# Kernel optimization log

Hardware: AMD Instinct MI355X
Metric: run time of the kernel (lower is better)

Reference implementation:

```python
import jax, jax.numpy as jnp
import numpy as np


def setup_inputs() -> dict:
    key = jax.random.key(0)
    k1, k2, k3 = jax.random.split(key, 3)
    B, C, Hg, Wg, Dg = 4, 12, 16, 16, 8
    H, W = 1024, 1024
    grid = jax.random.normal(k1, (B, C, Hg, Wg, Dg), dtype=jnp.float32)
    guide = jax.random.uniform(k2, (B, 1, H, W), dtype=jnp.float32)
    input_image = jax.random.normal(k3, (B, 3, H, W), dtype=jnp.float32)
    return {"grid": grid, "guide": guide, "input_image": input_image}


def reference(grid, guide, input_image):
    # grid: [B, C, Hg, Wg, Dg]; guide: [B,1,H,W]; input_image: [B,3,H,W]
    B, C, Hg, Wg, Dg = grid.shape
    H, W = input_image.shape[2], input_image.shape[3]
    dt = grid.dtype

    # depth coordinate from guide (matches torch: floor -> clamp, frac clamped to [0,1])
    g = guide[:, 0]                                   # [B,H,W]
    d_coords = g * (Dg - 1)
    d_lo = jnp.clip(jnp.floor(d_coords), 0, Dg - 1)
    d_lo_i = d_lo.astype(jnp.int32)
    d_hi_i = jnp.minimum(d_lo_i + 1, Dg - 1)
    d_w = jnp.clip(d_coords - d_lo, 0.0, 1.0)         # [B,H,W]

    # Spatial coords. NOTE: the torch code stacks [y, x] but grid_sample reads (x, y),
    # so row index i maps to the grid WIDTH axis and column j maps to the HEIGHT axis.
    # align_corners=True: x_pix = (x_norm+1)/2*(size-1).
    i_idx = jnp.arange(H, dtype=dt)
    j_idx = jnp.arange(W, dtype=dt)
    ww = i_idx / (H - 1) * (Wg - 1)                   # [H], width coord per row
    hh = j_idx / (W - 1) * (Hg - 1)                   # [W], height coord per col
    w0 = jnp.floor(ww).astype(jnp.int32)
    w1 = jnp.minimum(w0 + 1, Wg - 1)
    fw = ww - w0.astype(dt)                           # [H]
    h0 = jnp.floor(hh).astype(jnp.int32)
    h1 = jnp.minimum(h0 + 1, Hg - 1)
    fh = hh - h0.astype(dt)                           # [W]

    grid_t = jnp.transpose(grid, (0, 2, 3, 4, 1))     # [B,Hg,Wg,Dg,C]
    b = jnp.arange(B)[:, None, None]                  # [B,1,1]

    def corner(hI, wI, dI):
        # hI:[W] (col-dependent), wI:[H] (row-dependent), dI:[B,H,W]
        return grid_t[b, hI[None, None, :], wI[None, :, None], dI]  # [B,H,W,C]

    fh_b = fh[None, None, :, None]                    # [1,1,W,1]
    fw_b = fw[None, :, None, None]                    # [1,H,1,1]
    dw_b = d_w[..., None]                             # [B,H,W,1]

    out = jnp.zeros((B, H, W, C), dtype=dt)
    for hI, wh in ((h0, 1.0 - fh_b), (h1, fh_b)):
        for wI, wwt in ((w0, 1.0 - fw_b), (w1, fw_b)):
            for dI, wd in ((d_lo_i, 1.0 - dw_b), (d_hi_i, dw_b)):
                out = out + (wh * wwt * wd) * corner(hI, wI, dI)
    return jnp.transpose(out, (0, 3, 1, 2))           # [B,C,H,W]
```

## Files before the change

### kernel.cpp

```cpp
#include <hip/hip_runtime.h>

#define B_SZ 4
#define C_CH 12
#define H_G 16
#define W_G 16
#define D_G 8
#define H_IM 1024
#define W_IM 1024

#define QPITCH 9
#define QCSTRIDE (H_G * QPITCH)

__global__ __launch_bounds__(256) void bilateral_slice_kernel(
    const float* __restrict__ grid,
    const float* __restrict__ guide,
    float* __restrict__ out)
{
    __shared__ float2 Q[C_CH * QCSTRIDE];

    const int blk = blockIdx.x;
    const int b = blk >> 10;
    const int i = blk & 1023;
    const int t = threadIdx.x;

    const float wwv = ((float)i / 1023.0f) * 15.0f;
    const float w0f = floorf(wwv);
    const int   w0  = (int)w0f;
    const int   w1  = min(w0 + 1, W_G - 1);
    const float fw  = wwv - w0f;

    if (t < C_CH * H_G) {
        const int c = t >> 4;
        const int h = t & 15;
        const float* gp = grid +
            ((((size_t)b * C_CH + c) * H_G + h) * W_G + w0) * D_G;
        const int w1off = (w1 - w0) * D_G;
        const float4 a0 = *(const float4*)(gp);
        const float4 a1 = *(const float4*)(gp + 4);
        const float4 b0 = *(const float4*)(gp + w1off);
        const float4 b1 = *(const float4*)(gp + w1off + 4);
        float pd[8];
        pd[0] = a0.x + fw * (b0.x - a0.x);
        pd[1] = a0.y + fw * (b0.y - a0.y);
        pd[2] = a0.z + fw * (b0.z - a0.z);
        pd[3] = a0.w + fw * (b0.w - a0.w);
        pd[4] = a1.x + fw * (b1.x - a1.x);
        pd[5] = a1.y + fw * (b1.y - a1.y);
        pd[6] = a1.z + fw * (b1.z - a1.z);
        pd[7] = a1.w + fw * (b1.w - a1.w);
        float2* qrow = &Q[(c * H_G + h) * QPITCH];
        #pragma unroll
        for (int d = 0; d < 8; ++d) {
            const int dn = (d < 7) ? (d + 1) : 7;
            qrow[d] = make_float2(pd[d], pd[dn]);
        }
    }
    __syncthreads();

    const int j0 = t << 2;
    const float4 g4 = *(const float4*)(guide + (((size_t)b * H_IM) + i) * W_IM + j0);

    int   off0[4], off1[4];
    float dwv[4], fhv[4];
    const float* gv = (const float*)&g4;
    #pragma unroll
    for (int p = 0; p < 4; ++p) {
        const float dc  = gv[p] * 7.0f;
        float dlf = floorf(dc);
        dlf = fminf(fmaxf(dlf, 0.0f), 7.0f);
        const int dlo = (int)dlf;
        dwv[p] = fminf(fmaxf(dc - dlf, 0.0f), 1.0f);
        const int   j   = j0 + p;
        const float hhv = ((float)j / 1023.0f) * 15.0f;
        const float h0f = floorf(hhv);
        const int   h0  = (int)h0f;
        const int   h1  = min(h0 + 1, H_G - 1);
        fhv[p] = hhv - h0f;
        off0[p] = h0 * QPITCH + dlo;
        off1[p] = h1 * QPITCH + dlo;
    }

    float* outp = out + (((size_t)b * C_CH) * H_IM + i) * W_IM + j0;
    #pragma unroll
    for (int c = 0; c < C_CH; ++c) {
        const float2* Qc = &Q[c * QCSTRIDE];
        float4 o;
        float* ov = (float*)&o;
        #pragma unroll
        for (int p = 0; p < 4; ++p) {
            const float2 qa = Qc[off0[p]];
            const float2 qb = Qc[off1[p]];
            const float va = qa.x + dwv[p] * (qa.y - qa.x);
            const float vb = qb.x + dwv[p] * (qb.y - qb.x);
            ov[p] = va + fhv[p] * (vb - va);
        }
        *(float4*)(outp + (size_t)c * (H_IM * W_IM)) = o;
    }
}

extern "C" void kernel_launch(void* const* d_in, const int* in_sizes, int n_in,
                              void* d_out, int out_size, void* d_ws, size_t ws_size,
                              hipStream_t stream) {
    const float* grid  = (const float*)d_in[0];
    const float* guide = (const float*)d_in[1];
    float* out = (float*)d_out;

    const int nblocks = B_SZ * H_IM;
    bilateral_slice_kernel<<<nblocks, 256, 0, stream>>>(grid, guide, out);
}
```

Measured before the change: 250.6 us.

## Pack four interpolation corners per cell into float4 LDS and use nontemporal stores

The shared table is reorganized so each (h, d, channel) cell holds the four corner values (d, d+1, h, h+1) as one float4, with channels adjacent. One LDS read per channel per pixel replaces two float2 reads, and bilinear weights are precomputed once per pixel. Output writes become nontemporal stores to avoid polluting cache. The cost is more global loads in the table-build phase, a larger LDS footprint, and 48 live accumulator registers per thread.

```diff
diff --git a/kernel.cpp b/kernel.cpp
--- a/kernel.cpp
+++ b/kernel.cpp
@@ -8,15 +8,16 @@
 #define H_IM 1024
 #define W_IM 1024
 
-#define QPITCH 9
-#define QCSTRIDE (H_G * QPITCH)
+#define CELL_F4 13
+
+typedef float vfloat4 __attribute__((ext_vector_type(4)));
 
 __global__ __launch_bounds__(256) void bilateral_slice_kernel(
     const float* __restrict__ grid,
     const float* __restrict__ guide,
     float* __restrict__ out)
 {
-    __shared__ float2 Q[C_CH * QCSTRIDE];
+    __shared__ float4 Qs[H_G * D_G * CELL_F4];
 
     const int blk = blockIdx.x;
     const int b = blk >> 10;
@@ -30,71 +31,73 @@
     const float fw  = wwv - w0f;
 
     if (t < C_CH * H_G) {
-        const int c = t >> 4;
-        const int h = t & 15;
-        const float* gp = grid +
-            ((((size_t)b * C_CH + c) * H_G + h) * W_G + w0) * D_G;
-        const int w1off = (w1 - w0) * D_G;
-        const float4 a0 = *(const float4*)(gp);
-        const float4 a1 = *(const float4*)(gp + 4);
-        const float4 b0 = *(const float4*)(gp + w1off);
-        const float4 b1 = *(const float4*)(gp + w1off + 4);
-        float pd[8];
-        pd[0] = a0.x + fw * (b0.x - a0.x);
-        pd[1] = a0.y + fw * (b0.y - a0.y);
-        pd[2] = a0.z + fw * (b0.z - a0.z);
-        pd[3] = a0.w + fw * (b0.w - a0.w);
-        pd[4] = a1.x + fw * (b1.x - a1.x);
-        pd[5] = a1.y + fw * (b1.y - a1.y);
-        pd[6] = a1.z + fw * (b1.z - a1.z);
-        pd[7] = a1.w + fw * (b1.w - a1.w);
-        float2* qrow = &Q[(c * H_G + h) * QPITCH];
+        const int c  = t >> 4;
+        const int h  = t & 15;
+        const int h1 = min(h + 1, H_G - 1);
+        const float* r0 = grid + (((size_t)(b * C_CH + c) * H_G + h ) * W_G) * D_G;
+        const float* r1 = grid + (((size_t)(b * C_CH + c) * H_G + h1) * W_G) * D_G;
+        const int o0 = w0 * D_G;
+        const int o1 = w1 * D_G;
+        float A[8], Bv[8], Cv[8], Dv[8];
+        *(float4*)&A [0] = *(const float4*)(r0 + o0);
+        *(float4*)&A [4] = *(const float4*)(r0 + o0 + 4);
+        *(float4*)&Bv[0] = *(const float4*)(r0 + o1);
+        *(float4*)&Bv[4] = *(const float4*)(r0 + o1 + 4);
+        *(float4*)&Cv[0] = *(const float4*)(r1 + o0);
+        *(float4*)&Cv[4] = *(const float4*)(r1 + o0 + 4);
+        *(float4*)&Dv[0] = *(const float4*)(r1 + o1);
+        *(float4*)&Dv[4] = *(const float4*)(r1 + o1 + 4);
+        float P[8], P1[8];
         #pragma unroll
         for (int d = 0; d < 8; ++d) {
-            const int dn = (d < 7) ? (d + 1) : 7;
-            qrow[d] = make_float2(pd[d], pd[dn]);
+            P [d] = A [d] + fw * (Bv[d] - A [d]);
+            P1[d] = Cv[d] + fw * (Dv[d] - Cv[d]);
+        }
+        float4* cell = &Qs[(h * D_G) * CELL_F4 + c];
+        #pragma unroll
+        for (int d = 0; d < 8; ++d) {
+            const int dn = (d < 7) ? d + 1 : 7;
+            cell[d * CELL_F4] = make_float4(P[d], P[dn], P1[d], P1[dn]);
         }
     }
     __syncthreads();
 
     const int j0 = t << 2;
-    const float4 g4 = *(const float4*)(guide + (((size_t)b * H_IM) + i) * W_IM + j0);
+    const float4 g4 = *(const float4*)(guide + ((size_t)b * H_IM + i) * W_IM + j0);
+    const float* gv = (const float*)&g4;
 
-    int   off0[4], off1[4];
-    float dwv[4], fhv[4];
-    const float* gv = (const float*)&g4;
+    float o[C_CH][4];
     #pragma unroll
     for (int p = 0; p < 4; ++p) {
         const float dc  = gv[p] * 7.0f;
         float dlf = floorf(dc);
         dlf = fminf(fmaxf(dlf, 0.0f), 7.0f);
-        const int dlo = (int)dlf;
-        dwv[p] = fminf(fmaxf(dc - dlf, 0.0f), 1.0f);
+        const int   dlo = (int)dlf;
+        const float dw  = fminf(fmaxf(dc - dlf, 0.0f), 1.0f);
         const int   j   = j0 + p;
         const float hhv = ((float)j / 1023.0f) * 15.0f;
         const float h0f = floorf(hhv);
         const int   h0  = (int)h0f;
-        const int   h1  = min(h0 + 1, H_G - 1);
-        fhv[p] = hhv - h0f;
-        off0[p] = h0 * QPITCH + dlo;
-        off1[p] = h1 * QPITCH + dlo;
+        const float fh  = hhv - h0f;
+
+        const float wA = (1.0f - fh) * (1.0f - dw);
+        const float wB = (1.0f - fh) * dw;
+        const float wC = fh * (1.0f - dw);
+        const float wD = fh * dw;
+
+        const float4* cellp = &Qs[(h0 * D_G + dlo) * CELL_F4];
+        #pragma unroll
+        for (int c = 0; c < C_CH; ++c) {
+            const float4 q = cellp[c];
+            o[c][p] = wA * q.x + wB * q.y + wC * q.z + wD * q.w;
+        }
     }
 
     float* outp = out + (((size_t)b * C_CH) * H_IM + i) * W_IM + j0;
     #pragma unroll
     for (int c = 0; c < C_CH; ++c) {
-        const float2* Qc = &Q[c * QCSTRIDE];
-        float4 o;
-        float* ov = (float*)&o;
-        #pragma unroll
-        for (int p = 0; p < 4; ++p) {
-            const float2 qa = Qc[off0[p]];
-            const float2 qb = Qc[off1[p]];
-            const float va = qa.x + dwv[p] * (qa.y - qa.x);
-            const float vb = qb.x + dwv[p] * (qb.y - qb.x);
-            ov[p] = va + fhv[p] * (vb - va);
-        }
-        *(float4*)(outp + (size_t)c * (H_IM * W_IM)) = o;
+        vfloat4 v = { o[c][0], o[c][1], o[c][2], o[c][3] };
+        __builtin_nontemporal_store(v, (vfloat4*)(outp + (size_t)c * (H_IM * W_IM)));
     }
 }
 
```

Measured after the change: 247.7 us. No clear change (-1.1%).
